# Kernel tuning notes

Measured on AMD Instinct MI355X. Metric: run time of the kernel, lower is better.

Reference implementation:

```python
import jax, jax.numpy as jnp
import numpy as np

BATCH = 8192
EMBED_DIM = 256
INPUT_DIM = 3 * EMBED_DIM  # 768
NUM_LAYERS = 4
VOCAB_SIZES = [100000, 100000, 1000]
EPS = 1e-5


def setup_inputs() -> dict:
    key = jax.random.key(0)
    ks = jax.random.split(key, 20)
    inp = {}
    inp["x_p"] = jax.random.randint(ks[0], (BATCH,), 0, VOCAB_SIZES[0])
    inp["x_a"] = jax.random.randint(ks[1], (BATCH,), 0, VOCAB_SIZES[1])
    inp["x_c"] = jax.random.randint(ks[2], (BATCH,), 0, VOCAB_SIZES[2])
    inp["y_true"] = jax.random.uniform(ks[3], (BATCH, 1), dtype=jnp.float32)
    # embedding tables (nn.Embedding default init N(0,1))
    inp["E0"] = jax.random.normal(ks[4], (VOCAB_SIZES[0], EMBED_DIM), dtype=jnp.float32)
    inp["E1"] = jax.random.normal(ks[5], (VOCAB_SIZES[1], EMBED_DIM), dtype=jnp.float32)
    inp["E2"] = jax.random.normal(ks[6], (VOCAB_SIZES[2], EMBED_DIM), dtype=jnp.float32)
    lim = 1.0 / np.sqrt(INPUT_DIM)
    inp["Wd"] = jax.random.uniform(ks[7], (NUM_LAYERS, INPUT_DIM, INPUT_DIM), jnp.float32, -lim, lim)
    inp["bd"] = jnp.zeros((NUM_LAYERS, INPUT_DIM), jnp.float32)
    inp["Ws"] = jax.random.uniform(ks[8], (NUM_LAYERS, INPUT_DIM, INPUT_DIM), jnp.float32, -lim, lim)
    inp["bs"] = jnp.zeros((NUM_LAYERS, INPUT_DIM), jnp.float32)
    inp["wfd"] = jax.random.uniform(ks[9], (INPUT_DIM,), jnp.float32, -lim, lim)
    inp["bfd"] = jax.random.uniform(ks[10], (), jnp.float32, -lim, lim)
    inp["wfs"] = jax.random.uniform(ks[11], (INPUT_DIM,), jnp.float32, -lim, lim)
    inp["bfs"] = jax.random.uniform(ks[12], (), jnp.float32, -lim, lim)
    return inp


def _cross_network(x, W, b, net_id, mask_key):
    # per layer: cross = x @ W[l].T + b[l]; mask = bernoulli(sigmoid(layernorm over FULL tensor)); x += cross*mask
    for l in range(NUM_LAYERS):
        cross = jnp.einsum("bd,od->bo", x, W[l]) + b[l]
        m = jnp.mean(cross)
        v = jnp.mean(jnp.square(cross - m))  # F.layer_norm(x, x.size()): normalize over all elements
        ln = (cross - m) * jax.lax.rsqrt(v + EPS)
        p = jax.nn.sigmoid(ln)
        k = jax.random.fold_in(mask_key, net_id * NUM_LAYERS + l)
        mask = jax.random.bernoulli(k, p).astype(x.dtype)
        x = x + cross * mask
    return x


def _bce(p, y):
    return jnp.mean(-(y * jnp.log(p) + (1.0 - y) * jnp.log(1.0 - p)))


def reference(x_p, x_a, x_c, y_true, E0, E1, E2, Wd, bd, Ws, bs, wfd, bfd, wfs, bfs):
    h = EMBED_DIM // 2
    e0, e1, e2 = E0[x_p], E1[x_a], E2[x_c]  # [B, embed_dim] each
    e_a = jnp.concatenate([e0[:, :h], e1[:, :h], e2[:, :h]], axis=-1)
    e_b = jnp.concatenate([e0[:, h:], e1[:, h:], e2[:, h:]], axis=-1)
    x = jnp.concatenate([e_a, e_b], axis=-1)  # [B, 3*embed_dim]

    mask_key = jax.random.key(42)
    x_d = _cross_network(x, Wd, bd, 0, mask_key)
    x_s = _cross_network(x, Ws, bs, 1, mask_key)

    sd_d = jax.nn.sigmoid(x_d @ wfd + bfd)[:, None]  # fc_d(x_d)
    ss_s = jax.nn.sigmoid(x_s @ wfs + bfs)[:, None]  # fc_s(x_s)
    sd_s = jax.nn.sigmoid(x_s @ wfd + bfd)[:, None]  # fc_d(x_s)
    ss_d = jax.nn.sigmoid(x_d @ wfs + bfs)[:, None]  # fc_s(x_d)
    y_pred_d = 0.5 * (sd_d + ss_s)
    y_pred_s = 0.5 * (sd_s + ss_d)

    loss_d = _bce(y_pred_d, y_true)
    loss_s = _bce(y_pred_s, y_true)
    bce_loss = loss_d + loss_s
    weight_d = jnp.maximum(0.0, loss_d - bce_loss)
    weight_s = jnp.maximum(0.0, loss_s - bce_loss)
    tri_loss = bce_loss + weight_d * loss_d + weight_s * loss_s
    return (y_pred_d, tri_loss)
```

## Files before the change

kernel.cpp:

```cpp
#include <hip/hip_runtime.h>
#include <hip/hip_bf16.h>
#include <cstdint>
#include <cstddef>

#define BATCH   8192
#define DIM     768
#define NTOT    6291456
#define NLAYERS 4

typedef _Float16 half8 __attribute__((ext_vector_type(8)));
typedef float    f32x4 __attribute__((ext_vector_type(4)));

#define AS_GLOBAL __attribute__((address_space(1)))
#define AS_LDS    __attribute__((address_space(3)))

__device__ __forceinline__ void async_copy16(const void* g, void* l) {
  __builtin_amdgcn_global_load_lds((AS_GLOBAL const uint32_t*)g,
                                   (AS_LDS uint32_t*)l, 16, 0, 0);
}


__host__ __device__ __forceinline__ uint32_t rotl32(uint32_t v, int d) {
  return (v << d) | (v >> (32 - d));
}

__host__ __device__ __forceinline__ void threefry2x32(
    uint32_t k0, uint32_t k1, uint32_t x0, uint32_t x1,
    uint32_t& o0, uint32_t& o1) {
  uint32_t ks2 = k0 ^ k1 ^ 0x1BD11BDAu;
  x0 += k0; x1 += k1;
#define TF_R(r) { x0 += x1; x1 = rotl32(x1, (r)) ^ x0; }
  TF_R(13) TF_R(15) TF_R(26) TF_R(6)
  x0 += k1; x1 += ks2 + 1u;
  TF_R(17) TF_R(29) TF_R(16) TF_R(24)
  x0 += ks2; x1 += k0 + 2u;
  TF_R(13) TF_R(15) TF_R(26) TF_R(6)
  x0 += k0; x1 += k1 + 3u;
  TF_R(17) TF_R(29) TF_R(16) TF_R(24)
  x0 += k1; x1 += ks2 + 4u;
  TF_R(13) TF_R(15) TF_R(26) TF_R(6)
  x0 += ks2; x1 += k0 + 5u;
#undef TF_R
  o0 = x0; o1 = x1;
}

__device__ __forceinline__ double sigmoid_d(double x) {
  return 1.0 / (1.0 + exp(-x));
}

__device__ __forceinline__ double dexp(double x) {
  x = fmin(fmax(x, -708.0), 708.0);
  const double LOG2E = 1.4426950408889634;
  const double LN2   = 0.6931471805599453;
  double t = x * LOG2E;
  double n = rint(t);
  double g = (t - n) * LN2;
  double r = 2.7557319223985893e-07;
  r = r * g + 2.7557319223985888e-06;
  r = r * g + 2.4801587301587302e-05;
  r = r * g + 1.9841269841269841e-04;
  r = r * g + 1.3888888888888889e-03;
  r = r * g + 8.3333333333333332e-03;
  r = r * g + 4.1666666666666664e-02;
  r = r * g + 1.6666666666666666e-01;
  r = r * g + 0.5;
  r = r * g + 1.0;
  r = r * g + 1.0;
  int ni = (int)n;
  double sc = __longlong_as_double(((long long)(1023 + ni)) << 52);
  return r * sc;
}

__global__ __launch_bounds__(256) void gather_kernel(
    const int* __restrict__ x_p, const int* __restrict__ x_a,
    const int* __restrict__ x_c,
    const float* __restrict__ E0, const float* __restrict__ E1,
    const float* __restrict__ E2,
    _Float16* __restrict__ xdh, _Float16* __restrict__ xdl,
    _Float16* __restrict__ xsh, _Float16* __restrict__ xsl,
    double* __restrict__ stats, double* __restrict__ bce_acc) {
  if (blockIdx.x == 0 && threadIdx.x < 18) {
    if (threadIdx.x < 16) stats[threadIdx.x] = 0.0;
    else bce_acc[threadIdx.x - 16] = 0.0;
  }
  int gid = blockIdx.x * 256 + threadIdx.x;
  int g = gid >> 13;
  int b = gid & 8191;
  int f0 = g * 8;
  int half_ = f0 >= 384;
  int w = f0 - 384 * half_;
  int tbl = w >> 7;
  int c0 = (w & 127) + (half_ << 7);
  int row;
  const float* E;
  if (tbl == 0)      { E = E0; row = x_p[b]; }
  else if (tbl == 1) { E = E1; row = x_a[b]; }
  else               { E = E2; row = x_c[b]; }
  const float* src = &E[(size_t)row * 256 + c0];
  f32x4 v0 = *(const f32x4*)src;
  f32x4 v1 = *(const f32x4*)(src + 4);
  half8 h, l;
#pragma unroll
  for (int i = 0; i < 4; ++i) {
    h[i] = (_Float16)v0[i];
    l[i] = (_Float16)(v0[i] - (float)h[i]);
    h[i + 4] = (_Float16)v1[i];
    l[i + 4] = (_Float16)(v1[i] - (float)h[i + 4]);
  }
  size_t o = (size_t)gid * 8;
  *(half8*)&xdh[o] = h; *(half8*)&xdl[o] = l;
  *(half8*)&xsh[o] = h; *(half8*)&xsl[o] = l;
}

__global__ __launch_bounds__(256) void split_w_kernel(
    const float* __restrict__ Wd, const float* __restrict__ Ws,
    _Float16* __restrict__ Wh, _Float16* __restrict__ Wl) {
  int gid = blockIdx.x * 256 + threadIdx.x;
  int nl = gid / 73728;
  int r3 = gid - nl * 73728;
  int t  = r3 / 3072;
  int r4 = r3 - t * 3072;
  int kk = r4 / 768;
  int row = r4 - kk * 768;
  int k0 = t * 32 + kk * 8;
  const float* src = ((nl < 4) ? Wd : Ws) +
                     ((size_t)(nl & 3) * 768 + row) * 768 + k0;
  f32x4 v0 = *(const f32x4*)src;
  f32x4 v1 = *(const f32x4*)(src + 4);
  half8 h, l;
#pragma unroll
  for (int i = 0; i < 4; ++i) {
    h[i] = (_Float16)v0[i];
    l[i] = (_Float16)(v0[i] - (float)h[i]);
    h[i + 4] = (_Float16)v1[i];
    l[i + 4] = (_Float16)(v1[i] - (float)h[i + 4]);
  }
  size_t o = (size_t)gid * 8;
  *(half8*)&Wh[o] = h;
  *(half8*)&Wl[o] = l;
}

__global__ __launch_bounds__(512, 2) void gemm_mfma_kernel(
    const _Float16* __restrict__ xdh, const _Float16* __restrict__ xdl,
    const _Float16* __restrict__ xsh, const _Float16* __restrict__ xsl,
    const _Float16* __restrict__ Wh, const _Float16* __restrict__ Wl,
    const float* __restrict__ bd, const float* __restrict__ bs,
    float* __restrict__ crd, float* __restrict__ crs,
    double* __restrict__ stats, int layer) {
  const int net = blockIdx.z;
  const float* bias = (net ? bs : bd) + layer * DIM;
  float* C = net ? crs : crd;

  const int tid  = threadIdx.x;
  const int wave = tid >> 6, lane = tid & 63;
  const int quad = lane >> 4, l16 = lane & 15;
  const int m0 = blockIdx.x * 256;
  const int n0 = blockIdx.y * 192;

  __shared__ _Float16 lds[2 * 28672];

  const _Float16* xh = net ? xsh : xdh;
  const _Float16* xl = net ? xsl : xdl;
  const size_t wpanel = ((size_t)net * NLAYERS + layer) * (size_t)(24 * 4 * 768 * 8);
  const _Float16* wh = Wh + wpanel;
  const _Float16* wl = Wl + wpanel;

  const _Float16* gp[7];
  int gstr[7];
  int dbyte[7];
#pragma unroll
  for (int j = 0; j < 7; ++j) {
    int sb = wave * 448 + j * 64;
    dbyte[j] = sb * 16;
    int s = sb + lane;
    if (s < 2048) {
      int s2 = s & 1023;
      int kk = s2 >> 8, r = s2 & 255;
      gp[j] = ((s < 1024) ? xh : xl) + (size_t)(kk * 8192 + m0 + r) * 8;
      gstr[j] = 4 * 8192 * 8;
    } else {
      int s2 = s - 2048;
      int s3 = (s2 >= 768) ? s2 - 768 : s2;
      int kk = (s3 * 683) >> 17;
      int r  = s3 - kk * 192;
      gp[j] = ((s2 >= 768) ? wl : wh) + (size_t)(kk * 768 + n0 + r) * 8;
      gstr[j] = 4 * 768 * 8;
    }
  }

  const int wm = (wave >> 1) * 64;
  const int wn = (wave & 1) * 96;

  f32x4 acc[4][6];
#pragma unroll
  for (int i = 0; i < 4; ++i)
#pragma unroll
    for (int j = 0; j < 6; ++j) acc[i][j] = (f32x4){0.f, 0.f, 0.f, 0.f};

#pragma unroll
  for (int j = 0; j < 7; ++j)
    async_copy16(gp[j], (char*)lds + dbyte[j]);

  int cur = 0;
  for (int t = 0; t < 24; ++t) {
    __builtin_amdgcn_s_barrier();
    if (t < 23) {
#pragma unroll
      for (int j = 0; j < 7; ++j)
        async_copy16(gp[j] + (t + 1) * gstr[j],
                     (char*)lds + (cur ^ 1) * 57344 + dbyte[j]);
      asm volatile("s_waitcnt vmcnt(7)" ::: "memory");
    } else {
      asm volatile("s_waitcnt vmcnt(0)" ::: "memory");
    }
    __builtin_amdgcn_sched_barrier(0);
    __builtin_amdgcn_s_barrier();

    const _Float16* L = lds + cur * 28672;
    half8 ah[4], al[4], bh[2], bl[2];

#pragma unroll
    for (int mt = 0; mt < 4; ++mt) {
      int sl = quad * 256 + wm + mt * 16 + l16;
      ah[mt] = *(const half8*)&L[sl * 8];
      al[mt] = *(const half8*)&L[sl * 8 + 8192];
    }
#pragma unroll
    for (int nt = 0; nt < 2; ++nt) {
      int ss = 2048 + quad * 192 + wn + nt * 16 + l16;
      bh[nt] = *(const half8*)&L[ss * 8];
      bl[nt] = *(const half8*)&L[ss * 8 + 6144];
    }
    __builtin_amdgcn_s_barrier();
    __builtin_amdgcn_s_setprio(1);
#pragma unroll
    for (int nt = 0; nt < 2; ++nt)
#pragma unroll
      for (int mt = 0; mt < 4; ++mt) {
        f32x4 a = acc[mt][nt];
        a = __builtin_amdgcn_mfma_f32_16x16x32_f16(ah[mt], bh[nt], a, 0, 0, 0);
        a = __builtin_amdgcn_mfma_f32_16x16x32_f16(al[mt], bh[nt], a, 0, 0, 0);
        a = __builtin_amdgcn_mfma_f32_16x16x32_f16(ah[mt], bl[nt], a, 0, 0, 0);
        acc[mt][nt] = a;
      }
    __builtin_amdgcn_s_setprio(0);
    __builtin_amdgcn_s_barrier();

#pragma unroll
    for (int nt = 0; nt < 2; ++nt) {
      int ss = 2048 + quad * 192 + wn + (nt + 2) * 16 + l16;
      bh[nt] = *(const half8*)&L[ss * 8];
      bl[nt] = *(const half8*)&L[ss * 8 + 6144];
    }
    __builtin_amdgcn_s_barrier();
    __builtin_amdgcn_s_setprio(1);
#pragma unroll
    for (int nt = 0; nt < 2; ++nt)
#pragma unroll
      for (int mt = 0; mt < 4; ++mt) {
        f32x4 a = acc[mt][nt + 2];
        a = __builtin_amdgcn_mfma_f32_16x16x32_f16(ah[mt], bh[nt], a, 0, 0, 0);
        a = __builtin_amdgcn_mfma_f32_16x16x32_f16(al[mt], bh[nt], a, 0, 0, 0);
        a = __builtin_amdgcn_mfma_f32_16x16x32_f16(ah[mt], bl[nt], a, 0, 0, 0);
        acc[mt][nt + 2] = a;
      }
    __builtin_amdgcn_s_setprio(0);
    __builtin_amdgcn_s_barrier();

#pragma unroll
    for (int nt = 0; nt < 2; ++nt) {
      int ss = 2048 + quad * 192 + wn + (nt + 4) * 16 + l16;
      bh[nt] = *(const half8*)&L[ss * 8];
      bl[nt] = *(const half8*)&L[ss * 8 + 6144];
    }
    __builtin_amdgcn_s_barrier();
    __builtin_amdgcn_s_setprio(1);
#pragma unroll
    for (int nt = 0; nt < 2; ++nt)
#pragma unroll
      for (int mt = 0; mt < 4; ++mt) {
        f32x4 a = acc[mt][nt + 4];
        a = __builtin_amdgcn_mfma_f32_16x16x32_f16(ah[mt], bh[nt], a, 0, 0, 0);
        a = __builtin_amdgcn_mfma_f32_16x16x32_f16(al[mt], bh[nt], a, 0, 0, 0);
        a = __builtin_amdgcn_mfma_f32_16x16x32_f16(ah[mt], bl[nt], a, 0, 0, 0);
        acc[mt][nt + 4] = a;
      }
    __builtin_amdgcn_s_setprio(0);
    cur ^= 1;
  }

  __syncthreads();

  float biasv[6];
#pragma unroll
  for (int nt = 0; nt < 6; ++nt) biasv[nt] = bias[n0 + wn + nt * 16 + l16];

  double S = 0.0, Q = 0.0;
#pragma unroll
  for (int mt = 0; mt < 4; ++mt) {
#pragma unroll
    for (int nt = 0; nt < 6; ++nt) {
      int n = n0 + wn + nt * 16 + l16;
      size_t gbase = (size_t)(n >> 4) * 131072;
#pragma unroll
      for (int r = 0; r < 4; ++r) {
        int m = m0 + wm + mt * 16 + quad * 4 + r;
        float v = acc[mt][nt][r] + biasv[nt];
        C[gbase + m * 16 + l16] = v;
        S += (double)v;
        Q += (double)v * (double)v;
      }
    }
  }
#pragma unroll
  for (int off = 32; off > 0; off >>= 1) {
    S += __shfl_down(S, off);
    Q += __shfl_down(Q, off);
  }
  double* red = (double*)lds;
  if (lane == 0) { red[wave * 2] = S; red[wave * 2 + 1] = Q; }
  __syncthreads();
  if (tid == 0) {
    double s2 = 0.0, q2 = 0.0;
#pragma unroll
    for (int wv = 0; wv < 8; ++wv) { s2 += red[wv * 2]; q2 += red[wv * 2 + 1]; }
    double* st = stats + ((size_t)layer * 2 + net) * 2;
    atomicAdd(&st[0], s2);
    atomicAdd(&st[1], q2);
  }
}

__global__ __launch_bounds__(256) void mask_update_kernel(
    _Float16* __restrict__ xdh, _Float16* __restrict__ xdl,
    _Float16* __restrict__ xsh, _Float16* __restrict__ xsl,
    const float* __restrict__ crd, const float* __restrict__ crs,
    const double* __restrict__ stats, int layer,
    uint32_t kd0, uint32_t kd1, uint32_t ks0, uint32_t ks1) {
  const int net = blockIdx.y;
  _Float16* xh = net ? xsh : xdh;
  _Float16* xl = net ? xsl : xdl;
  const float* cr = net ? crs : crd;
  const uint32_t k0 = net ? ks0 : kd0;
  const uint32_t k1 = net ? ks1 : kd1;

  const double invN = 1.0 / (double)NTOT;
  const double* st = stats + ((size_t)layer * 2 + net) * 2;
  double meand = st[0] * invN;
  double vard  = st[1] * invN - meand * meand;
  float m  = (float)meand;
  float sv = (float)vard + 1e-5f;
  float rs = (float)(1.0 / sqrt((double)sv));

  int cg = blockIdx.x * 256 + threadIdx.x;
  int g16 = cg >> 13;
  int b   = cg & 8191;
  int f0  = g16 * 16;

  f32x4 c4[4];
#pragma unroll
  for (int i = 0; i < 4; ++i) c4[i] = *(const f32x4*)&cr[(size_t)cg * 16 + i * 4];

  size_t xg0 = ((size_t)g16 * 2) * 8192 + b;
  half8 h0 = *(const half8*)&xh[xg0 * 8];
  half8 l0 = *(const half8*)&xl[xg0 * 8];
  half8 h1 = *(const half8*)&xh[(xg0 + 8192) * 8];
  half8 l1 = *(const half8*)&xl[(xg0 + 8192) * 8];
  half8 ho0, lo0, ho1, lo1;

#pragma unroll
  for (int i = 0; i < 16; ++i) {
    float c  = c4[i >> 2][i & 3];
    float ln = (c - m) * rs;
    uint32_t o0, o1;
    threefry2x32(k0, k1, 0u, (uint32_t)(b * 768 + f0 + i), o0, o1);
    uint32_t bits = o0 ^ o1;
    float u = __uint_as_float(0x3F800000u | (bits >> 9)) - 1.0f;
    double e  = dexp(-(double)ln);
    double ue = (double)u;
    float xv = (i < 8) ? ((float)h0[i & 7] + (float)l0[i & 7])
                       : ((float)h1[i & 7] + (float)l1[i & 7]);
    if (ue + ue * e < 1.0) xv += c;
    _Float16 hh = (_Float16)xv;
    _Float16 ll = (_Float16)(xv - (float)hh);
    if (i < 8) { ho0[i & 7] = hh; lo0[i & 7] = ll; }
    else       { ho1[i & 7] = hh; lo1[i & 7] = ll; }
  }
  *(half8*)&xh[xg0 * 8] = ho0;
  *(half8*)&xl[xg0 * 8] = lo0;
  *(half8*)&xh[(xg0 + 8192) * 8] = ho1;
  *(half8*)&xl[(xg0 + 8192) * 8] = lo1;
}

__global__ __launch_bounds__(256) void head_kernel(
    const _Float16* __restrict__ xdh, const _Float16* __restrict__ xdl,
    const _Float16* __restrict__ xsh, const _Float16* __restrict__ xsl,
    const float* __restrict__ wfd, const float* __restrict__ wfs,
    const float* __restrict__ bfd_p, const float* __restrict__ bfs_p,
    const float* __restrict__ y_true,
    float* __restrict__ out, double* __restrict__ bce_acc) {
  const int tq = threadIdx.x >> 6;
  const int tb = threadIdx.x & 63;
  const int row = blockIdx.x * 64 + tb;

  float dd = 0.f, dsw = 0.f, sd = 0.f, ssw = 0.f;
  const int g0 = tq * 24;
  for (int g = g0; g < g0 + 24; ++g) {
    size_t o = ((size_t)g * 8192 + row) * 8;
    half8 hd = *(const half8*)&xdh[o];
    half8 ld = *(const half8*)&xdl[o];
    half8 hs = *(const half8*)&xsh[o];
    half8 ls = *(const half8*)&xsl[o];
#pragma unroll
    for (int i = 0; i < 8; ++i) {
      float vd = (float)hd[i] + (float)ld[i];
      float vs = (float)hs[i] + (float)ls[i];
      float wd = wfd[g * 8 + i], ws = wfs[g * 8 + i];
      dd  = fmaf(vd, wd, dd);
      dsw = fmaf(vd, ws, dsw);
      sd  = fmaf(vs, wd, sd);
      ssw = fmaf(vs, ws, ssw);
    }
  }
  __shared__ float part[4][64][4];
  part[tq][tb][0] = dd;  part[tq][tb][1] = dsw;
  part[tq][tb][2] = sd;  part[tq][tb][3] = ssw;
  __syncthreads();

  if (threadIdx.x < 64) {
    float DD  = part[0][tb][0] + part[1][tb][0] + part[2][tb][0] + part[3][tb][0];
    float DSW = part[0][tb][1] + part[1][tb][1] + part[2][tb][1] + part[3][tb][1];
    float SD  = part[0][tb][2] + part[1][tb][2] + part[2][tb][2] + part[3][tb][2];
    float SSW = part[0][tb][3] + part[1][tb][3] + part[2][tb][3] + part[3][tb][3];
    float bfd = *bfd_p, bfs = *bfs_p;
    double sdd = sigmoid_d((double)(DD + bfd));
    double ssd = sigmoid_d((double)(DSW + bfs));
    double sds = sigmoid_d((double)(SD + bfd));
    double sss = sigmoid_d((double)(SSW + bfs));
    double ypd = 0.5 * (sdd + sss);
    double yps = 0.5 * (sds + ssd);
    out[row] = (float)ypd;
    double y = (double)y_true[row];
    double bce_d = -(y * log(ypd) + (1.0 - y) * log(1.0 - ypd));
    double bce_s = -(y * log(yps) + (1.0 - y) * log(1.0 - yps));
#pragma unroll
    for (int off = 32; off > 0; off >>= 1) {
      bce_d += __shfl_down(bce_d, off);
      bce_s += __shfl_down(bce_s, off);
    }
    if (tb == 0) {
      atomicAdd(&bce_acc[0], bce_d);
      atomicAdd(&bce_acc[1], bce_s);
    }
  }
}

__global__ void loss_kernel(const double* __restrict__ bce_acc,
                            float* __restrict__ out_tri) {
  if (threadIdx.x == 0) {
    double loss_d = bce_acc[0] / (double)BATCH;
    double loss_s = bce_acc[1] / (double)BATCH;
    double bce = loss_d + loss_s;
    double wd = fmax(0.0, loss_d - bce);
    double ws = fmax(0.0, loss_s - bce);
    out_tri[0] = (float)(bce + wd * loss_d + ws * loss_s);
  }
}

extern "C" void kernel_launch(void* const* d_in, const int* in_sizes, int n_in,
                              void* d_out, int out_size, void* d_ws, size_t ws_size,
                              hipStream_t stream) {
  const int* x_p = (const int*)d_in[0];
  const int* x_a = (const int*)d_in[1];
  const int* x_c = (const int*)d_in[2];
  const float* y_true = (const float*)d_in[3];
  const float* E0 = (const float*)d_in[4];
  const float* E1 = (const float*)d_in[5];
  const float* E2 = (const float*)d_in[6];
  const float* Wd = (const float*)d_in[7];
  const float* bd = (const float*)d_in[8];
  const float* Ws = (const float*)d_in[9];
  const float* bs = (const float*)d_in[10];
  const float* wfd = (const float*)d_in[11];
  const float* bfd = (const float*)d_in[12];
  const float* wfs = (const float*)d_in[13];
  const float* bfs = (const float*)d_in[14];
  float* out = (float*)d_out;

  char* p = (char*)d_ws;
  float* crd = (float*)p;                 p += (size_t)NTOT * 4;
  float* crs = (float*)p;                 p += (size_t)NTOT * 4;
  double* stats   = (double*)p;           p += (size_t)16 * 8;
  double* bce_acc = (double*)p;           p += (size_t)2 * 8;
  _Float16* xdh = (_Float16*)p;           p += (size_t)NTOT * 2;
  _Float16* xdl = (_Float16*)p;           p += (size_t)NTOT * 2;
  _Float16* xsh = (_Float16*)p;           p += (size_t)NTOT * 2;
  _Float16* xsl = (_Float16*)p;           p += (size_t)NTOT * 2;
  _Float16* Wh  = (_Float16*)p;           p += (size_t)2 * NLAYERS * DIM * DIM * 2;
  _Float16* Wl  = (_Float16*)p;           p += (size_t)2 * NLAYERS * DIM * DIM * 2;

  gather_kernel<<<NTOT / 8 / 256, 256, 0, stream>>>(
      x_p, x_a, x_c, E0, E1, E2, xdh, xdl, xsh, xsl, stats, bce_acc);
  split_w_kernel<<<2 * NLAYERS * DIM * DIM / 8 / 256, 256, 0, stream>>>(
      Wd, Ws, Wh, Wl);

  for (int l = 0; l < NLAYERS; ++l) {
    gemm_mfma_kernel<<<dim3(32, 4, 2), 512, 0, stream>>>(
        xdh, xdl, xsh, xsl, Wh, Wl, bd, bs, crd, crs, stats, l);
    uint32_t kd0, kd1, ks0, ks1;
    threefry2x32(0u, 42u, 0u, (uint32_t)l, kd0, kd1);
    threefry2x32(0u, 42u, 0u, (uint32_t)(4 + l), ks0, ks1);
    mask_update_kernel<<<dim3(NTOT / 16 / 256, 2), 256, 0, stream>>>(
        xdh, xdl, xsh, xsl, crd, crs, stats, l, kd0, kd1, ks0, ks1);
  }

  head_kernel<<<BATCH / 64, 256, 0, stream>>>(
      xdh, xdl, xsh, xsl, wfd, wfs, bfd, bfs, y_true, out, bce_acc);
  loss_kernel<<<1, 64, 0, stream>>>(bce_acc, out + BATCH);
}
```

Before: 643.5 us.

## Fuse cross GEMM and mask update into one cooperative per-layer kernel

Each layer's GEMM kernel and its separate mask/update kernel are merged into one cooperative kernel. A grid-wide sync separates them, because the layer-norm statistics need the global sum over all elements. After the sync, each block stages its accumulator tile in LDS and applies the bias, layer-norm, threefry Bernoulli mask and residual update directly to the split-fp16 x buffers. This drops the full fp32 cross buffers and their global write and read-back each layer, and halves the kernel launches. In exchange it needs a cooperative launch with all blocks co-resident, and the mask phase now runs on only the GEMM's block count with a grid barrier in every layer.

```diff
diff --git a/kernel.cpp b/kernel.cpp
--- a/kernel.cpp
+++ b/kernel.cpp
@@ -1,7 +1,10 @@
 #include <hip/hip_runtime.h>
 #include <hip/hip_bf16.h>
+#include <hip/hip_cooperative_groups.h>
 #include <cstdint>
 #include <cstddef>
+
+namespace cg = cooperative_groups;
 
 #define BATCH   8192
 #define DIM     768
@@ -140,16 +143,15 @@
   *(half8*)&Wl[o] = l;
 }
 
-__global__ __launch_bounds__(512, 2) void gemm_mfma_kernel(
-    const _Float16* __restrict__ xdh, const _Float16* __restrict__ xdl,
-    const _Float16* __restrict__ xsh, const _Float16* __restrict__ xsl,
+__global__ __launch_bounds__(512, 2) void layer_kernel(
+    _Float16* __restrict__ xdh, _Float16* __restrict__ xdl,
+    _Float16* __restrict__ xsh, _Float16* __restrict__ xsl,
     const _Float16* __restrict__ Wh, const _Float16* __restrict__ Wl,
     const float* __restrict__ bd, const float* __restrict__ bs,
-    float* __restrict__ crd, float* __restrict__ crs,
-    double* __restrict__ stats, int layer) {
+    double* __restrict__ stats, int layer,
+    uint32_t kd0, uint32_t kd1, uint32_t ks0, uint32_t ks1) {
   const int net = blockIdx.z;
   const float* bias = (net ? bs : bd) + layer * DIM;
-  float* C = net ? crs : crd;
 
   const int tid  = threadIdx.x;
   const int wave = tid >> 6, lane = tid & 63;
@@ -159,8 +161,8 @@
 
   __shared__ _Float16 lds[2 * 28672];
 
-  const _Float16* xh = net ? xsh : xdh;
-  const _Float16* xl = net ? xsl : xdl;
+  _Float16* xh = net ? xsh : xdh;
+  _Float16* xl = net ? xsl : xdl;
   const size_t wpanel = ((size_t)net * NLAYERS + layer) * (size_t)(24 * 4 * 768 * 8);
   const _Float16* wh = Wh + wpanel;
   const _Float16* wl = Wl + wpanel;
@@ -176,7 +178,8 @@
     if (s < 2048) {
       int s2 = s & 1023;
       int kk = s2 >> 8, r = s2 & 255;
-      gp[j] = ((s < 1024) ? xh : xl) + (size_t)(kk * 8192 + m0 + r) * 8;
+      gp[j] = ((s < 1024) ? (const _Float16*)xh : (const _Float16*)xl) +
+              (size_t)(kk * 8192 + m0 + r) * 8;
       gstr[j] = 4 * 8192 * 8;
     } else {
       int s2 = s - 2048;
@@ -297,21 +300,15 @@
 
   double S = 0.0, Q = 0.0;
 #pragma unroll
-  for (int mt = 0; mt < 4; ++mt) {
-#pragma unroll
-    for (int nt = 0; nt < 6; ++nt) {
-      int n = n0 + wn + nt * 16 + l16;
-      size_t gbase = (size_t)(n >> 4) * 131072;
+  for (int mt = 0; mt < 4; ++mt)
+#pragma unroll
+    for (int nt = 0; nt < 6; ++nt)
 #pragma unroll
       for (int r = 0; r < 4; ++r) {
-        int m = m0 + wm + mt * 16 + quad * 4 + r;
         float v = acc[mt][nt][r] + biasv[nt];
-        C[gbase + m * 16 + l16] = v;
         S += (double)v;
         Q += (double)v * (double)v;
       }
-    }
-  }
 #pragma unroll
   for (int off = 32; off > 0; off >>= 1) {
     S += __shfl_down(S, off);
@@ -320,75 +317,81 @@
   double* red = (double*)lds;
   if (lane == 0) { red[wave * 2] = S; red[wave * 2 + 1] = Q; }
   __syncthreads();
+  double* st = stats + ((size_t)layer * 2 + net) * 2;
   if (tid == 0) {
     double s2 = 0.0, q2 = 0.0;
 #pragma unroll
     for (int wv = 0; wv < 8; ++wv) { s2 += red[wv * 2]; q2 += red[wv * 2 + 1]; }
-    double* st = stats + ((size_t)layer * 2 + net) * 2;
     atomicAdd(&st[0], s2);
     atomicAdd(&st[1], q2);
   }
-}
-
-__global__ __launch_bounds__(256) void mask_update_kernel(
-    _Float16* __restrict__ xdh, _Float16* __restrict__ xdl,
-    _Float16* __restrict__ xsh, _Float16* __restrict__ xsl,
-    const float* __restrict__ crd, const float* __restrict__ crs,
-    const double* __restrict__ stats, int layer,
-    uint32_t kd0, uint32_t kd1, uint32_t ks0, uint32_t ks1) {
-  const int net = blockIdx.y;
-  _Float16* xh = net ? xsh : xdh;
-  _Float16* xl = net ? xsl : xdl;
-  const float* cr = net ? crs : crd;
-  const uint32_t k0 = net ? ks0 : kd0;
-  const uint32_t k1 = net ? ks1 : kd1;
-
+  __threadfence();
+
+  cg::this_grid().sync();
+
+  if (tid == 0) {
+    red[0] = atomicAdd(&st[0], 0.0);
+    red[1] = atomicAdd(&st[1], 0.0);
+  }
+  __syncthreads();
   const double invN = 1.0 / (double)NTOT;
-  const double* st = stats + ((size_t)layer * 2 + net) * 2;
-  double meand = st[0] * invN;
-  double vard  = st[1] * invN - meand * meand;
-  float m  = (float)meand;
+  double meand = red[0] * invN;
+  double vard  = red[1] * invN - meand * meand;
+  float mF = (float)meand;
   float sv = (float)vard + 1e-5f;
   float rs = (float)(1.0 / sqrt((double)sv));
 
-  int cg = blockIdx.x * 256 + threadIdx.x;
-  int g16 = cg >> 13;
-  int b   = cg & 8191;
-  int f0  = g16 * 16;
-
-  f32x4 c4[4];
-#pragma unroll
-  for (int i = 0; i < 4; ++i) c4[i] = *(const f32x4*)&cr[(size_t)cg * 16 + i * 4];
-
-  size_t xg0 = ((size_t)g16 * 2) * 8192 + b;
-  half8 h0 = *(const half8*)&xh[xg0 * 8];
-  half8 l0 = *(const half8*)&xl[xg0 * 8];
-  half8 h1 = *(const half8*)&xh[(xg0 + 8192) * 8];
-  half8 l1 = *(const half8*)&xl[(xg0 + 8192) * 8];
-  half8 ho0, lo0, ho1, lo1;
-
-#pragma unroll
-  for (int i = 0; i < 16; ++i) {
-    float c  = c4[i >> 2][i & 3];
-    float ln = (c - m) * rs;
-    uint32_t o0, o1;
-    threefry2x32(k0, k1, 0u, (uint32_t)(b * 768 + f0 + i), o0, o1);
-    uint32_t bits = o0 ^ o1;
-    float u = __uint_as_float(0x3F800000u | (bits >> 9)) - 1.0f;
-    double e  = dexp(-(double)ln);
-    double ue = (double)u;
-    float xv = (i < 8) ? ((float)h0[i & 7] + (float)l0[i & 7])
-                       : ((float)h1[i & 7] + (float)l1[i & 7]);
-    if (ue + ue * e < 1.0) xv += c;
-    _Float16 hh = (_Float16)xv;
-    _Float16 ll = (_Float16)(xv - (float)hh);
-    if (i < 8) { ho0[i & 7] = hh; lo0[i & 7] = ll; }
-    else       { ho1[i & 7] = hh; lo1[i & 7] = ll; }
-  }
-  *(half8*)&xh[xg0 * 8] = ho0;
-  *(half8*)&xl[xg0 * 8] = lo0;
-  *(half8*)&xh[(xg0 + 8192) * 8] = ho1;
-  *(half8*)&xl[(xg0 + 8192) * 8] = lo1;
+  const uint32_t K0 = net ? ks0 : kd0;
+  const uint32_t K1 = net ? ks1 : kd1;
+  float* Ct = (float*)lds;
+  const int rl  = tid & 255;
+  const int gp2 = tid >> 8;
+  const int b = m0 + rl;
+
+  for (int cgp = 0; cgp < 2; ++cgp) {
+    __syncthreads();
+    if ((wave & 1) == cgp) {
+#pragma unroll
+      for (int mt = 0; mt < 4; ++mt)
+#pragma unroll
+        for (int nt = 0; nt < 6; ++nt) {
+          int nl = nt * 16 + l16;
+#pragma unroll
+          for (int r = 0; r < 4; ++r) {
+            int ml = wm + mt * 16 + quad * 4 + r;
+            Ct[ml * 97 + nl] = acc[mt][nt][r] + biasv[nt];
+          }
+        }
+    }
+    __syncthreads();
+    for (int gi = 0; gi < 6; ++gi) {
+      int gc = gp2 + gi * 2;
+      int g  = (n0 >> 3) + cgp * 12 + gc;
+      int fbase = g * 8;
+      size_t xo = ((size_t)g * 8192 + b) * 8;
+      half8 hx = *(const half8*)&xh[xo];
+      half8 lx = *(const half8*)&xl[xo];
+      half8 ho, lo;
+#pragma unroll
+      for (int i = 0; i < 8; ++i) {
+        float c  = Ct[rl * 97 + gc * 8 + i];
+        float ln = (c - mF) * rs;
+        uint32_t o0, o1;
+        threefry2x32(K0, K1, 0u, (uint32_t)(b * 768 + fbase + i), o0, o1);
+        uint32_t bits = o0 ^ o1;
+        float u = __uint_as_float(0x3F800000u | (bits >> 9)) - 1.0f;
+        double e  = dexp(-(double)ln);
+        double ue = (double)u;
+        float xv = (float)hx[i] + (float)lx[i];
+        if (ue + ue * e < 1.0) xv += c;
+        _Float16 hh = (_Float16)xv;
+        ho[i] = hh;
+        lo[i] = (_Float16)(xv - (float)hh);
+      }
+      *(half8*)&xh[xo] = ho;
+      *(half8*)&xl[xo] = lo;
+    }
+  }
 }
 
 __global__ __launch_bounds__(256) void head_kernel(
@@ -487,8 +490,6 @@
   float* out = (float*)d_out;
 
   char* p = (char*)d_ws;
-  float* crd = (float*)p;                 p += (size_t)NTOT * 4;
-  float* crs = (float*)p;                 p += (size_t)NTOT * 4;
   double* stats   = (double*)p;           p += (size_t)16 * 8;
   double* bce_acc = (double*)p;           p += (size_t)2 * 8;
   _Float16* xdh = (_Float16*)p;           p += (size_t)NTOT * 2;
@@ -504,13 +505,14 @@
       Wd, Ws, Wh, Wl);
 
   for (int l = 0; l < NLAYERS; ++l) {
-    gemm_mfma_kernel<<<dim3(32, 4, 2), 512, 0, stream>>>(
-        xdh, xdl, xsh, xsl, Wh, Wl, bd, bs, crd, crs, stats, l);
     uint32_t kd0, kd1, ks0, ks1;
     threefry2x32(0u, 42u, 0u, (uint32_t)l, kd0, kd1);
     threefry2x32(0u, 42u, 0u, (uint32_t)(4 + l), ks0, ks1);
-    mask_update_kernel<<<dim3(NTOT / 16 / 256, 2), 256, 0, stream>>>(
-        xdh, xdl, xsh, xsl, crd, crs, stats, l, kd0, kd1, ks0, ks1);
+    int lay = l;
+    void* args[] = {&xdh, &xdl, &xsh, &xsl, &Wh, &Wl, &bd, &bs,
+                    &stats, &lay, &kd0, &kd1, &ks0, &ks1};
+    hipLaunchCooperativeKernel((const void*)layer_kernel, dim3(32, 4, 2),
+                               dim3(512), args, 0, stream);
   }
 
   head_kernel<<<BATCH / 64, 256, 0, stream>>>(
```

New measurement: 972.3 us. 51.1% more time.
